# Kernel tuning notes

Hardware: AMD Instinct MI355X
Metric: run time of the kernel (lower is better)

## Reference

```python
import jax, jax.numpy as jnp
import numpy as np

E, F, H = 8, 5632, 2048
T = 8192


def setup_inputs() -> dict:
    key = jax.random.key(0)
    k1, k2, k3, k4 = jax.random.split(key, 4)
    s_w = 1.0 / np.sqrt(H)
    return {
        "expert_idx": 3,
        "hidden_states": jax.random.normal(k1, (T, H), dtype=jnp.float32),
        "fc1_1": jax.random.normal(k2, (E, F, H), dtype=jnp.float32) * s_w,
        "fc1_2": jax.random.normal(k3, (E, F, H), dtype=jnp.float32) * s_w,
        "fc2": jax.random.normal(k4, (E, H, F), dtype=jnp.float32) * (1.0 / np.sqrt(F)),
    }


def reference(expert_idx, hidden_states, fc1_1, fc1_2, fc2):
    # Select this expert's weights: [F,H], [F,H], [H,F]
    w1 = fc1_1[expert_idx]
    w2 = fc1_2[expert_idx]
    w3 = fc2[expert_idx]
    # SwiGLU FFN: silu(x @ w1^T) * (x @ w2^T) @ w3^T
    gate = jnp.einsum("th,fh->tf", hidden_states, w1)
    up = jnp.einsum("th,fh->tf", hidden_states, w2)
    fc1_out = jax.nn.silu(gate) * up  # [T, F]
    out = jnp.einsum("tf,hf->th", fc1_out, w3)  # [T, H]
    return out
```

## Files before the change

### kernel.cpp

```cpp
#include <hip/hip_runtime.h>
#include <hip/hip_bf16.h>

#define T_DIM 8192
#define H_DIM 2048
#define F_DIM 5632

typedef __attribute__((ext_vector_type(4))) float f32x4;
typedef __attribute__((ext_vector_type(8))) short bf16x8;

static __device__ __forceinline__ void gload16(const void* g, void* l) {
    __builtin_amdgcn_global_load_lds(
        (const __attribute__((address_space(1))) void*)g,
        (__attribute__((address_space(3))) void*)l,
        16, 0, 0);
}

static __device__ __forceinline__ unsigned short f2bf(float f) {
    unsigned int u = __float_as_uint(f);
    u += 0x7fffu + ((u >> 16) & 1u);
    return (unsigned short)(u >> 16);
}

__global__ __launch_bounds__(256)
void cvt_x(const float* __restrict__ src, unsigned short* __restrict__ dst, long n)
{
    const long stride = (long)gridDim.x * blockDim.x;
    for (long i = (long)blockIdx.x * blockDim.x + threadIdx.x; i * 4 < n; i += stride) {
        const float4 v = *(const float4*)(src + i * 4);
        ushort4 o;
        o.x = f2bf(v.x); o.y = f2bf(v.y); o.z = f2bf(v.z); o.w = f2bf(v.w);
        *(ushort4*)(dst + i * 4) = o;
    }
}

__global__ __launch_bounds__(256)
void cvt_w(const float* __restrict__ w1, const float* __restrict__ w2,
           const float* __restrict__ w3, const int* __restrict__ eidx,
           unsigned short* __restrict__ W12, unsigned short* __restrict__ W3b)
{
    const long seg = (long)F_DIM * H_DIM;
    const long e   = (long)(*eidx);
    const long nchunks = 3 * seg / 4;
    const long stride = (long)gridDim.x * blockDim.x;
    for (long i = (long)blockIdx.x * blockDim.x + threadIdx.x; i < nchunks; i += stride) {
        const long t = i * 4;
        const int  s = (int)(t / seg);
        const long o = t - (long)s * seg;
        const float4 v = *(const float4*)((s == 0 ? w1 : s == 1 ? w2 : w3) + e * seg + o);
        ushort4 ov;
        ov.x = f2bf(v.x); ov.y = f2bf(v.y); ov.z = f2bf(v.z); ov.w = f2bf(v.w);
        if (s == 2) {
            *(ushort4*)(W3b + o) = ov;
        } else {
            const long r   = o >> 11;
            const long col = o & 2047;
            const long R   = (r >> 4) * 32 + (r & 15) + (s == 1 ? 16 : 0);
            *(ushort4*)(W12 + R * 2048 + col) = ov;
        }
    }
}

static __device__ __forceinline__ void stage_half(const unsigned short* __restrict__ g,
                                                  long grow0, long ldk, long kb,
                                                  unsigned short* l, int t, int i0)
{
    const int r  = t >> 3;
    const int cc = ((t & 7) ^ (r & 7)) << 3;
    #pragma unroll
    for (int ii = i0; ii < i0 + 2; ++ii)
        gload16(g + (grow0 + ii * 64 + r) * ldk + kb + cc,
                l + ii * 4096 + t * 8);
}

static __device__ __forceinline__ bf16x8 ldsfrag(const unsigned short* base,
                                                 int row, int kk, int q)
{
    return *(const bf16x8*)(base + row * 64 + (((kk * 4 + q) ^ (row & 7)) << 3));
}

__global__ __launch_bounds__(512, 4)
void gemm_fc1(const unsigned short* __restrict__ X,
              const unsigned short* __restrict__ W12,
              unsigned short* __restrict__ Hout)
{
    constexpr int NK = H_DIM / 64;

    __shared__ __align__(16) unsigned short sAll[40960];

    const int tid  = threadIdx.x;
    const int lane = tid & 63;
    const int wid  = tid >> 6;
    const int wm   = wid >> 2;
    const int wn   = wid & 3;
    const int q    = lane >> 4;
    const int lr   = lane & 15;

    const int bid = blockIdx.x;
    const int x   = bid & 7;
    const int ii  = bid >> 3;
    const int bn  = ii >> 2;
    const int bm  = x * 4 + (ii & 3);

    const long arow0 = (long)bm * 256;
    const long brow0 = (long)bn * 128;

    unsigned short* sB = sAll + 32768;

    f32x4 acc[8][2] = {};

    stage_half(X,   arow0, H_DIM, 0, sAll, tid, 0);
    stage_half(X,   arow0, H_DIM, 0, sAll, tid, 2);
    stage_half(W12, brow0, H_DIM, 0, sB,   tid, 0);

    for (int j = 0; j < NK; ++j) {
        unsigned short* la = sAll + (j & 1) * 16384;

        if (j + 1 < NK) {
            unsigned short* na = sAll + ((j + 1) & 1) * 16384;
            stage_half(X, arow0, H_DIM, (long)(j + 1) * 64, na, tid, 0);
            stage_half(X, arow0, H_DIM, (long)(j + 1) * 64, na, tid, 2);
            asm volatile("s_waitcnt vmcnt(4)" ::: "memory");
        } else {
            asm volatile("s_waitcnt vmcnt(0)" ::: "memory");
        }
        __builtin_amdgcn_s_barrier();

        bf16x8 bf[2][2];
        #pragma unroll
        for (int nb = 0; nb < 2; ++nb)
            #pragma unroll
            for (int kk = 0; kk < 2; ++kk)
                bf[nb][kk] = ldsfrag(sB, wn * 32 + nb * 16 + lr, kk, q);

        bf16x8 af0[4][2];
        #pragma unroll
        for (int mi = 0; mi < 4; ++mi)
            #pragma unroll
            for (int kk = 0; kk < 2; ++kk)
                af0[mi][kk] = ldsfrag(la, wm * 128 + mi * 16 + lr, kk, q);
        __builtin_amdgcn_s_barrier();
        __builtin_amdgcn_s_setprio(1);
        #pragma unroll
        for (int mi = 0; mi < 4; ++mi)
            #pragma unroll
            for (int nb = 0; nb < 2; ++nb)
                #pragma unroll
                for (int kk = 0; kk < 2; ++kk)
                    acc[mi][nb] = __builtin_amdgcn_mfma_f32_16x16x32_bf16(
                        af0[mi][kk], bf[nb][kk], acc[mi][nb], 0, 0, 0);
        __builtin_amdgcn_s_setprio(0);

        bf16x8 af1[4][2];
        #pragma unroll
        for (int mi = 0; mi < 4; ++mi)
            #pragma unroll
            for (int kk = 0; kk < 2; ++kk)
                af1[mi][kk] = ldsfrag(la, wm * 128 + (mi + 4) * 16 + lr, kk, q);
        if (j + 1 < NK)
            stage_half(W12, brow0, H_DIM, (long)(j + 1) * 64, sB, tid, 0);
        __builtin_amdgcn_s_barrier();
        __builtin_amdgcn_s_setprio(1);
        #pragma unroll
        for (int mi = 0; mi < 4; ++mi)
            #pragma unroll
            for (int nb = 0; nb < 2; ++nb)
                #pragma unroll
                for (int kk = 0; kk < 2; ++kk)
                    acc[mi + 4][nb] = __builtin_amdgcn_mfma_f32_16x16x32_bf16(
                        af1[mi][kk], bf[nb][kk], acc[mi + 4][nb], 0, 0, 0);
        __builtin_amdgcn_s_setprio(0);
    }

    const long orow = (long)bm * 256 + wm * 128;
    const long ocol = (long)bn * 64 + wn * 16 + lr;
    #pragma unroll
    for (int mi = 0; mi < 8; ++mi)
        #pragma unroll
        for (int r = 0; r < 4; ++r) {
            const float g = acc[mi][0][r];
            const float u = acc[mi][1][r];
            const float h = __fdividef(g, 1.0f + __expf(-g)) * u;
            Hout[(orow + mi * 16 + q * 4 + r) * (long)F_DIM + ocol] = f2bf(h);
        }
}

#define PHASE_BODY(p, STAGE_STMT)                                              \
    {                                                                          \
        bf16x8 af[2][2];                                                       \
        _Pragma("unroll")                                                      \
        for (int l_ = 0; l_ < 2; ++l_)                                         \
            _Pragma("unroll")                                                  \
            for (int kk = 0; kk < 2; ++kk)                                     \
                af[l_][kk] = ldsfrag(la, wm * 128 + (p) * 32 + l_ * 16 + lr, kk, q); \
        STAGE_STMT;                                                            \
        __builtin_amdgcn_s_barrier();                                          \
        __builtin_amdgcn_s_setprio(1);                                         \
        _Pragma("unroll")                                                      \
        for (int l_ = 0; l_ < 2; ++l_)                                         \
            _Pragma("unroll")                                                  \
            for (int ni = 0; ni < 4; ++ni)                                     \
                _Pragma("unroll")                                              \
                for (int kk = 0; kk < 2; ++kk)                                 \
                    acc[(p) * 2 + l_][ni] = __builtin_amdgcn_mfma_f32_16x16x32_bf16( \
                        af[l_][kk], bf[ni][kk], acc[(p) * 2 + l_][ni], 0, 0, 0);     \
        __builtin_amdgcn_s_setprio(0);                                         \
        __builtin_amdgcn_s_barrier();                                          \
    }

__global__ __launch_bounds__(512, 2)
void gemm_out(const unsigned short* __restrict__ A,
              const unsigned short* __restrict__ B,
              float* __restrict__ Out)
{
    constexpr int NK  = F_DIM / 64;
    constexpr int NBN = H_DIM / 256;

    __shared__ __align__(16) unsigned short sAll[4 * 16384];

    const int tid  = threadIdx.x;
    const int lane = tid & 63;
    const int wid  = tid >> 6;
    const int wm   = wid >> 2;
    const int wn   = wid & 3;
    const int q    = lane >> 4;
    const int lr   = lane & 15;

    const int nwg = gridDim.x;
    const int bid = blockIdx.x;
    const int cpx = nwg >> 3;
    const int swz = (bid & 7) * cpx + (bid >> 3);
    const int bm  = swz / NBN;
    const int bn  = swz % NBN;

    const long arow0 = (long)bm * 256;
    const long brow0 = (long)bn * 256;

    f32x4 acc[8][4] = {};

    stage_half(A, arow0, F_DIM, 0,  sAll,          tid, 0);
    stage_half(A, arow0, F_DIM, 0,  sAll,          tid, 2);
    stage_half(B, brow0, F_DIM, 0,  sAll + 16384,  tid, 0);
    stage_half(B, brow0, F_DIM, 0,  sAll + 16384,  tid, 2);
    stage_half(B, brow0, F_DIM, 64, sAll + 49152,  tid, 0);
    stage_half(B, brow0, F_DIM, 64, sAll + 49152,  tid, 2);

    for (int j = 0; j < NK; ++j) {
        unsigned short* la = sAll + (j & 1) * 32768;
        unsigned short* lb = la + 16384;

        if (j + 1 < NK) {
            unsigned short* na = sAll + ((j + 1) & 1) * 32768;
            stage_half(A, arow0, F_DIM, (long)(j + 1) * 64, na, tid, 0);
            stage_half(A, arow0, F_DIM, (long)(j + 1) * 64, na, tid, 2);
            asm volatile("s_waitcnt vmcnt(8)" ::: "memory");
        } else {
            asm volatile("s_waitcnt vmcnt(0)" ::: "memory");
        }
        __builtin_amdgcn_s_barrier();

        bf16x8 bf[4][2];
        #pragma unroll
        for (int ni = 0; ni < 4; ++ni)
            #pragma unroll
            for (int kk = 0; kk < 2; ++kk)
                bf[ni][kk] = ldsfrag(lb, wn * 64 + ni * 16 + lr, kk, q);

        PHASE_BODY(0, {})
        PHASE_BODY(1, { if (j + 2 < NK) stage_half(B, brow0, F_DIM, (long)(j + 2) * 64, lb, tid, 0); })
        PHASE_BODY(2, { if (j + 2 < NK) stage_half(B, brow0, F_DIM, (long)(j + 2) * 64, lb, tid, 2); })
        PHASE_BODY(3, {})
    }

    const long orow = (long)bm * 256 + wm * 128;
    const long ocol = (long)bn * 256 + wn * 64;
    #pragma unroll
    for (int mi = 0; mi < 8; ++mi)
        #pragma unroll
        for (int ni = 0; ni < 4; ++ni)
            #pragma unroll
            for (int r = 0; r < 4; ++r)
                Out[(orow + mi * 16 + q * 4 + r) * (long)H_DIM + (ocol + ni * 16 + lr)]
                    = acc[mi][ni][r];
}

extern "C" void kernel_launch(void* const* d_in, const int* in_sizes, int n_in,
                              void* d_out, int out_size, void* d_ws, size_t ws_size,
                              hipStream_t stream)
{
    const int*   eidx = (const int*)d_in[0];
    const float* x    = (const float*)d_in[1];
    const float* w1   = (const float*)d_in[2];
    const float* w2   = (const float*)d_in[3];
    const float* w3   = (const float*)d_in[4];
    float* out = (float*)d_out;

    const size_t SZ_X = (size_t)T_DIM * H_DIM;
    const size_t SZ_W = (size_t)F_DIM * H_DIM;

    unsigned short* Xb  = (unsigned short*)d_ws;
    unsigned short* W12 = Xb  + SZ_X;
    unsigned short* W3b = W12 + 2 * SZ_W;
    unsigned short* Hb  = W3b + SZ_W;

    cvt_x<<<2048, 256, 0, stream>>>(x, Xb, (long)SZ_X);
    cvt_w<<<2048, 256, 0, stream>>>(w1, w2, w3, eidx, W12, W3b);

    gemm_fc1<<<2816, 512, 0, stream>>>(Xb, W12, Hb);
    gemm_out<<<(T_DIM / 256) * (H_DIM / 256), 512, 0, stream>>>(Hb, W3b, out);
}
```

Measured before the change: 545.8 us.

## Reshape fc1 GEMM tile to 128x256 with wider B tile per wave

Changes the fc1 gate/up GEMM block tile from 256 rows of X by 128 interleaved weight rows to 128 rows of X by 256 weight rows. Each wave now computes a 64x64 sub-tile instead of 128x32, and shared memory drops from 80KB to 64KB. The block-index mapping, staging counts and wait counts are adjusted to match, and extra barriers are added after each MFMA phase. The aim is a more square per-wave tile, better LDS fragment reuse and higher occupancy. The added barriers and the changed grid mapping could cost synchronisation time and L2 locality.

```diff
diff --git a/kernel.cpp b/kernel.cpp
--- a/kernel.cpp
+++ b/kernel.cpp
@@ -85,7 +85,7 @@
 {
     constexpr int NK = H_DIM / 64;
 
-    __shared__ __align__(16) unsigned short sAll[40960];
+    __shared__ __align__(16) unsigned short sAll[32768];
 
     const int tid  = threadIdx.x;
     const int lane = tid & 63;
@@ -98,90 +98,100 @@
     const int bid = blockIdx.x;
     const int x   = bid & 7;
     const int ii  = bid >> 3;
-    const int bn  = ii >> 2;
-    const int bm  = x * 4 + (ii & 3);
-
-    const long arow0 = (long)bm * 256;
-    const long brow0 = (long)bn * 128;
-
-    unsigned short* sB = sAll + 32768;
-
-    f32x4 acc[8][2] = {};
+    const int bn  = ii >> 3;
+    const int bm  = x * 8 + (ii & 7);
+
+    const long arow0 = (long)bm * 128;
+    const long brow0 = (long)bn * 256;
+
+    unsigned short* sB = sAll + 16384;
+
+    f32x4 acc[4][4] = {};
 
     stage_half(X,   arow0, H_DIM, 0, sAll, tid, 0);
-    stage_half(X,   arow0, H_DIM, 0, sAll, tid, 2);
     stage_half(W12, brow0, H_DIM, 0, sB,   tid, 0);
+    stage_half(W12, brow0, H_DIM, 0, sB,   tid, 2);
 
     for (int j = 0; j < NK; ++j) {
-        unsigned short* la = sAll + (j & 1) * 16384;
+        unsigned short* la = sAll + (j & 1) * 8192;
 
         if (j + 1 < NK) {
-            unsigned short* na = sAll + ((j + 1) & 1) * 16384;
+            unsigned short* na = sAll + ((j + 1) & 1) * 8192;
             stage_half(X, arow0, H_DIM, (long)(j + 1) * 64, na, tid, 0);
-            stage_half(X, arow0, H_DIM, (long)(j + 1) * 64, na, tid, 2);
-            asm volatile("s_waitcnt vmcnt(4)" ::: "memory");
+            asm volatile("s_waitcnt vmcnt(2)" ::: "memory");
         } else {
             asm volatile("s_waitcnt vmcnt(0)" ::: "memory");
         }
         __builtin_amdgcn_s_barrier();
 
-        bf16x8 bf[2][2];
+        bf16x8 bf[4][2];
         #pragma unroll
-        for (int nb = 0; nb < 2; ++nb)
+        for (int nf = 0; nf < 4; ++nf)
             #pragma unroll
             for (int kk = 0; kk < 2; ++kk)
-                bf[nb][kk] = ldsfrag(sB, wn * 32 + nb * 16 + lr, kk, q);
-
-        bf16x8 af0[4][2];
-        #pragma unroll
-        for (int mi = 0; mi < 4; ++mi)
-            #pragma unroll
-            for (int kk = 0; kk < 2; ++kk)
-                af0[mi][kk] = ldsfrag(la, wm * 128 + mi * 16 + lr, kk, q);
-        __builtin_amdgcn_s_barrier();
-        __builtin_amdgcn_s_setprio(1);
-        #pragma unroll
-        for (int mi = 0; mi < 4; ++mi)
-            #pragma unroll
-            for (int nb = 0; nb < 2; ++nb)
+                bf[nf][kk] = ldsfrag(sB, wn * 64 + nf * 16 + lr, kk, q);
+
+        {
+            bf16x8 af[2][2];
+            #pragma unroll
+            for (int mi = 0; mi < 2; ++mi)
                 #pragma unroll
                 for (int kk = 0; kk < 2; ++kk)
-                    acc[mi][nb] = __builtin_amdgcn_mfma_f32_16x16x32_bf16(
-                        af0[mi][kk], bf[nb][kk], acc[mi][nb], 0, 0, 0);
-        __builtin_amdgcn_s_setprio(0);
-
-        bf16x8 af1[4][2];
-        #pragma unroll
-        for (int mi = 0; mi < 4; ++mi)
-            #pragma unroll
-            for (int kk = 0; kk < 2; ++kk)
-                af1[mi][kk] = ldsfrag(la, wm * 128 + (mi + 4) * 16 + lr, kk, q);
-        if (j + 1 < NK)
-            stage_half(W12, brow0, H_DIM, (long)(j + 1) * 64, sB, tid, 0);
-        __builtin_amdgcn_s_barrier();
-        __builtin_amdgcn_s_setprio(1);
-        #pragma unroll
-        for (int mi = 0; mi < 4; ++mi)
-            #pragma unroll
-            for (int nb = 0; nb < 2; ++nb)
+                    af[mi][kk] = ldsfrag(la, wm * 64 + mi * 16 + lr, kk, q);
+            __builtin_amdgcn_s_barrier();
+            __builtin_amdgcn_s_setprio(1);
+            #pragma unroll
+            for (int mi = 0; mi < 2; ++mi)
+                #pragma unroll
+                for (int nf = 0; nf < 4; ++nf)
+                    #pragma unroll
+                    for (int kk = 0; kk < 2; ++kk)
+                        acc[mi][nf] = __builtin_amdgcn_mfma_f32_16x16x32_bf16(
+                            af[mi][kk], bf[nf][kk], acc[mi][nf], 0, 0, 0);
+            __builtin_amdgcn_s_setprio(0);
+            __builtin_amdgcn_s_barrier();
+        }
+
+        {
+            bf16x8 af[2][2];
+            #pragma unroll
+            for (int mi = 0; mi < 2; ++mi)
                 #pragma unroll
                 for (int kk = 0; kk < 2; ++kk)
-                    acc[mi + 4][nb] = __builtin_amdgcn_mfma_f32_16x16x32_bf16(
-                        af1[mi][kk], bf[nb][kk], acc[mi + 4][nb], 0, 0, 0);
-        __builtin_amdgcn_s_setprio(0);
-    }
-
-    const long orow = (long)bm * 256 + wm * 128;
-    const long ocol = (long)bn * 64 + wn * 16 + lr;
+                    af[mi][kk] = ldsfrag(la, wm * 64 + (mi + 2) * 16 + lr, kk, q);
+            if (j + 1 < NK) {
+                stage_half(W12, brow0, H_DIM, (long)(j + 1) * 64, sB, tid, 0);
+                stage_half(W12, brow0, H_DIM, (long)(j + 1) * 64, sB, tid, 2);
+            }
+            __builtin_amdgcn_s_barrier();
+            __builtin_amdgcn_s_setprio(1);
+            #pragma unroll
+            for (int mi = 0; mi < 2; ++mi)
+                #pragma unroll
+                for (int nf = 0; nf < 4; ++nf)
+                    #pragma unroll
+                    for (int kk = 0; kk < 2; ++kk)
+                        acc[mi + 2][nf] = __builtin_amdgcn_mfma_f32_16x16x32_bf16(
+                            af[mi][kk], bf[nf][kk], acc[mi + 2][nf], 0, 0, 0);
+            __builtin_amdgcn_s_setprio(0);
+            __builtin_amdgcn_s_barrier();
+        }
+    }
+
+    const long orow = (long)bm * 128 + wm * 64;
+    const long ocolb = (long)bn * 128 + wn * 32;
     #pragma unroll
-    for (int mi = 0; mi < 8; ++mi)
+    for (int mi = 0; mi < 4; ++mi)
         #pragma unroll
-        for (int r = 0; r < 4; ++r) {
-            const float g = acc[mi][0][r];
-            const float u = acc[mi][1][r];
-            const float h = __fdividef(g, 1.0f + __expf(-g)) * u;
-            Hout[(orow + mi * 16 + q * 4 + r) * (long)F_DIM + ocol] = f2bf(h);
-        }
+        for (int nj = 0; nj < 2; ++nj)
+            #pragma unroll
+            for (int r = 0; r < 4; ++r) {
+                const float g = acc[mi][2 * nj][r];
+                const float u = acc[mi][2 * nj + 1][r];
+                const float h = __fdividef(g, 1.0f + __expf(-g)) * u;
+                Hout[(orow + mi * 16 + q * 4 + r) * (long)F_DIM +
+                     (ocolb + nj * 16 + lr)] = f2bf(h);
+            }
 }
 
 #define PHASE_BODY(p, STAGE_STMT)                                              \
```

Result: no change. 553.5 us (+1.4%).

## Switch fc1 GEMM to 32x32x16 MFMA with 4x2 wave layout

Applied to the files above, without the earlier changes.

The fc1 gate/up GEMM now uses 32x32x16 bf16 MFMA tiles instead of 16x16x32, and the eight waves are rearranged as a 4x2 grid, each owning 64 rows by 64 interleaved gate/up columns. The W12 interleave is widened from 16-row to 32-row groups so that each 32-column fragment pair lines up as gate and up for the fused SiLU epilogue. Larger MFMA tiles need fewer LDS fragment reads per FLOP and fewer MFMA issues. The cost is a different accumulator register layout, an extra barrier after each phase, and possibly more register pressure.

```diff
diff --git a/kernel.cpp b/kernel.cpp
--- a/kernel.cpp
+++ b/kernel.cpp
@@ -5,8 +5,9 @@
 #define H_DIM 2048
 #define F_DIM 5632
 
-typedef __attribute__((ext_vector_type(4))) float f32x4;
-typedef __attribute__((ext_vector_type(8))) short bf16x8;
+typedef __attribute__((ext_vector_type(4)))  float f32x4;
+typedef __attribute__((ext_vector_type(16))) float f32x16;
+typedef __attribute__((ext_vector_type(8)))  short bf16x8;
 
 static __device__ __forceinline__ void gload16(const void* g, void* l) {
     __builtin_amdgcn_global_load_lds(
@@ -54,7 +55,7 @@
         } else {
             const long r   = o >> 11;
             const long col = o & 2047;
-            const long R   = (r >> 4) * 32 + (r & 15) + (s == 1 ? 16 : 0);
+            const long R   = (r >> 5) * 64 + (r & 31) + (s == 1 ? 32 : 0);
             *(ushort4*)(W12 + R * 2048 + col) = ov;
         }
     }
@@ -72,10 +73,16 @@
                 l + ii * 4096 + t * 8);
 }
 
+static __device__ __forceinline__ bf16x8 ldsfragc(const unsigned short* base,
+                                                  int row, int c)
+{
+    return *(const bf16x8*)(base + row * 64 + ((c ^ (row & 7)) << 3));
+}
+
 static __device__ __forceinline__ bf16x8 ldsfrag(const unsigned short* base,
                                                  int row, int kk, int q)
 {
-    return *(const bf16x8*)(base + row * 64 + (((kk * 4 + q) ^ (row & 7)) << 3));
+    return ldsfragc(base, row, kk * 4 + q);
 }
 
 __global__ __launch_bounds__(512, 4)
@@ -90,10 +97,10 @@
     const int tid  = threadIdx.x;
     const int lane = tid & 63;
     const int wid  = tid >> 6;
-    const int wm   = wid >> 2;
-    const int wn   = wid & 3;
-    const int q    = lane >> 4;
-    const int lr   = lane & 15;
+    const int wm   = wid >> 1;
+    const int wn   = wid & 1;
+    const int l5   = lane & 31;
+    const int h    = lane >> 5;
 
     const int bid = blockIdx.x;
     const int x   = bid & 7;
@@ -106,7 +113,7 @@
 
     unsigned short* sB = sAll + 32768;
 
-    f32x4 acc[8][2] = {};
+    f32x16 acc[2][2] = {};
 
     stage_half(X,   arow0, H_DIM, 0, sAll, tid, 0);
     stage_half(X,   arow0, H_DIM, 0, sAll, tid, 2);
@@ -125,63 +132,63 @@
         }
         __builtin_amdgcn_s_barrier();
 
-        bf16x8 bf[2][2];
+        bf16x8 bf[2][4];
         #pragma unroll
-        for (int nb = 0; nb < 2; ++nb)
-            #pragma unroll
-            for (int kk = 0; kk < 2; ++kk)
-                bf[nb][kk] = ldsfrag(sB, wn * 32 + nb * 16 + lr, kk, q);
-
-        bf16x8 af0[4][2];
+        for (int nf = 0; nf < 2; ++nf)
+            #pragma unroll
+            for (int s = 0; s < 4; ++s)
+                bf[nf][s] = ldsfragc(sB, wn * 64 + nf * 32 + l5, s * 2 + h);
+
+        {
+            bf16x8 af[4];
+            #pragma unroll
+            for (int s = 0; s < 4; ++s)
+                af[s] = ldsfragc(la, wm * 64 + l5, s * 2 + h);
+            __builtin_amdgcn_s_barrier();
+            __builtin_amdgcn_s_setprio(1);
+            #pragma unroll
+            for (int nf = 0; nf < 2; ++nf)
+                #pragma unroll
+                for (int s = 0; s < 4; ++s)
+                    acc[0][nf] = __builtin_amdgcn_mfma_f32_32x32x16_bf16(
+                        af[s], bf[nf][s], acc[0][nf], 0, 0, 0);
+            __builtin_amdgcn_s_setprio(0);
+            __builtin_amdgcn_s_barrier();
+        }
+
+        {
+            bf16x8 af[4];
+            #pragma unroll
+            for (int s = 0; s < 4; ++s)
+                af[s] = ldsfragc(la, wm * 64 + 32 + l5, s * 2 + h);
+            if (j + 1 < NK)
+                stage_half(W12, brow0, H_DIM, (long)(j + 1) * 64, sB, tid, 0);
+            __builtin_amdgcn_s_barrier();
+            __builtin_amdgcn_s_setprio(1);
+            #pragma unroll
+            for (int nf = 0; nf < 2; ++nf)
+                #pragma unroll
+                for (int s = 0; s < 4; ++s)
+                    acc[1][nf] = __builtin_amdgcn_mfma_f32_32x32x16_bf16(
+                        af[s], bf[nf][s], acc[1][nf], 0, 0, 0);
+            __builtin_amdgcn_s_setprio(0);
+            __builtin_amdgcn_s_barrier();
+        }
+    }
+
+    const long col = (long)bn * 64 + wn * 32 + l5;
+    #pragma unroll
+    for (int mi = 0; mi < 2; ++mi) {
+        const long rowb = (long)bm * 256 + wm * 64 + mi * 32 + 4 * h;
         #pragma unroll
-        for (int mi = 0; mi < 4; ++mi)
-            #pragma unroll
-            for (int kk = 0; kk < 2; ++kk)
-                af0[mi][kk] = ldsfrag(la, wm * 128 + mi * 16 + lr, kk, q);
-        __builtin_amdgcn_s_barrier();
-        __builtin_amdgcn_s_setprio(1);
-        #pragma unroll
-        for (int mi = 0; mi < 4; ++mi)
-            #pragma unroll
-            for (int nb = 0; nb < 2; ++nb)
-                #pragma unroll
-                for (int kk = 0; kk < 2; ++kk)
-                    acc[mi][nb] = __builtin_amdgcn_mfma_f32_16x16x32_bf16(
-                        af0[mi][kk], bf[nb][kk], acc[mi][nb], 0, 0, 0);
-        __builtin_amdgcn_s_setprio(0);
-
-        bf16x8 af1[4][2];
-        #pragma unroll
-        for (int mi = 0; mi < 4; ++mi)
-            #pragma unroll
-            for (int kk = 0; kk < 2; ++kk)
-                af1[mi][kk] = ldsfrag(la, wm * 128 + (mi + 4) * 16 + lr, kk, q);
-        if (j + 1 < NK)
-            stage_half(W12, brow0, H_DIM, (long)(j + 1) * 64, sB, tid, 0);
-        __builtin_amdgcn_s_barrier();
-        __builtin_amdgcn_s_setprio(1);
-        #pragma unroll
-        for (int mi = 0; mi < 4; ++mi)
-            #pragma unroll
-            for (int nb = 0; nb < 2; ++nb)
-                #pragma unroll
-                for (int kk = 0; kk < 2; ++kk)
-                    acc[mi + 4][nb] = __builtin_amdgcn_mfma_f32_16x16x32_bf16(
-                        af1[mi][kk], bf[nb][kk], acc[mi + 4][nb], 0, 0, 0);
-        __builtin_amdgcn_s_setprio(0);
-    }
-
-    const long orow = (long)bm * 256 + wm * 128;
-    const long ocol = (long)bn * 64 + wn * 16 + lr;
-    #pragma unroll
-    for (int mi = 0; mi < 8; ++mi)
-        #pragma unroll
-        for (int r = 0; r < 4; ++r) {
-            const float g = acc[mi][0][r];
-            const float u = acc[mi][1][r];
-            const float h = __fdividef(g, 1.0f + __expf(-g)) * u;
-            Hout[(orow + mi * 16 + q * 4 + r) * (long)F_DIM + ocol] = f2bf(h);
-        }
+        for (int reg = 0; reg < 16; ++reg) {
+            const long row = rowb + (reg & 3) + 8 * (reg >> 2);
+            const float g = acc[mi][0][reg];
+            const float u = acc[mi][1][reg];
+            const float hv = __fdividef(g, 1.0f + __expf(-g)) * u;
+            Hout[row * (long)F_DIM + col] = f2bf(hv);
+        }
+    }
 }
 
 #define PHASE_BODY(p, STAGE_STMT)                                              \
```

Result: slower. 657.9 us (+20.5%).

## Enlarge fc1 block tile to 256x256 with 1024 threads and double-buffered B

Applied to the files above, without the earlier changes.

The fused gate/up GEMM now uses 16 waves per block and a 256x256 output tile, doubling the weight rows per block and halving the grid. Both the X and W12 tiles are double-buffered in LDS, and the loads for the next K step are issued together. This replaces the old single-buffered B with its mid-iteration reload and extra barriers, leaving one barrier per K step. The aim is more operand reuse per LDS byte and less synchronization. The cost is 128 KB of LDS per block, which limits residency to one block per CU, plus coarser scheduling with fewer blocks.

```diff
diff --git a/kernel.cpp b/kernel.cpp
--- a/kernel.cpp
+++ b/kernel.cpp
@@ -72,26 +72,35 @@
                 l + ii * 4096 + t * 8);
 }
 
+static __device__ __forceinline__ void stage_q(const unsigned short* __restrict__ g,
+                                               long grow0, long ldk, long kb,
+                                               unsigned short* l, int t)
+{
+    const int r  = t >> 3;
+    const int cc = ((t & 7) ^ (r & 7)) << 3;
+    gload16(g + (grow0 + r) * ldk + kb + cc, l + t * 8);
+}
+
 static __device__ __forceinline__ bf16x8 ldsfrag(const unsigned short* base,
                                                  int row, int kk, int q)
 {
     return *(const bf16x8*)(base + row * 64 + (((kk * 4 + q) ^ (row & 7)) << 3));
 }
 
-__global__ __launch_bounds__(512, 4)
+__global__ __launch_bounds__(1024, 4)
 void gemm_fc1(const unsigned short* __restrict__ X,
               const unsigned short* __restrict__ W12,
               unsigned short* __restrict__ Hout)
 {
     constexpr int NK = H_DIM / 64;
 
-    __shared__ __align__(16) unsigned short sAll[40960];
+    __shared__ __align__(16) unsigned short sAll[65536];
 
     const int tid  = threadIdx.x;
     const int lane = tid & 63;
     const int wid  = tid >> 6;
-    const int wm   = wid >> 2;
-    const int wn   = wid & 3;
+    const int wm   = wid >> 3;
+    const int wn   = wid & 7;
     const int q    = lane >> 4;
     const int lr   = lane & 15;
 
@@ -102,23 +111,30 @@
     const int bm  = x * 4 + (ii & 3);
 
     const long arow0 = (long)bm * 256;
-    const long brow0 = (long)bn * 128;
-
-    unsigned short* sB = sAll + 32768;
+    const long brow0 = (long)bn * 256;
+
+    unsigned short* bufA = sAll;
+    unsigned short* bufB = sAll + 32768;
 
     f32x4 acc[8][2] = {};
 
-    stage_half(X,   arow0, H_DIM, 0, sAll, tid, 0);
-    stage_half(X,   arow0, H_DIM, 0, sAll, tid, 2);
-    stage_half(W12, brow0, H_DIM, 0, sB,   tid, 0);
+    stage_q(X,   arow0,       H_DIM, 0, bufA,        tid);
+    stage_q(X,   arow0 + 128, H_DIM, 0, bufA + 8192, tid);
+    stage_q(W12, brow0,       H_DIM, 0, bufB,        tid);
+    stage_q(W12, brow0 + 128, H_DIM, 0, bufB + 8192, tid);
 
     for (int j = 0; j < NK; ++j) {
-        unsigned short* la = sAll + (j & 1) * 16384;
+        unsigned short* la = bufA + (j & 1) * 16384;
+        unsigned short* lb = bufB + (j & 1) * 16384;
 
         if (j + 1 < NK) {
-            unsigned short* na = sAll + ((j + 1) & 1) * 16384;
-            stage_half(X, arow0, H_DIM, (long)(j + 1) * 64, na, tid, 0);
-            stage_half(X, arow0, H_DIM, (long)(j + 1) * 64, na, tid, 2);
+            unsigned short* na = bufA + ((j + 1) & 1) * 16384;
+            unsigned short* nb = bufB + ((j + 1) & 1) * 16384;
+            const long kbn = (long)(j + 1) * 64;
+            stage_q(X,   arow0,       H_DIM, kbn, na,        tid);
+            stage_q(X,   arow0 + 128, H_DIM, kbn, na + 8192, tid);
+            stage_q(W12, brow0,       H_DIM, kbn, nb,        tid);
+            stage_q(W12, brow0 + 128, H_DIM, kbn, nb + 8192, tid);
             asm volatile("s_waitcnt vmcnt(4)" ::: "memory");
         } else {
             asm volatile("s_waitcnt vmcnt(0)" ::: "memory");
@@ -127,52 +143,52 @@
 
         bf16x8 bf[2][2];
         #pragma unroll
-        for (int nb = 0; nb < 2; ++nb)
+        for (int nb_ = 0; nb_ < 2; ++nb_)
             #pragma unroll
             for (int kk = 0; kk < 2; ++kk)
-                bf[nb][kk] = ldsfrag(sB, wn * 32 + nb * 16 + lr, kk, q);
-
-        bf16x8 af0[4][2];
-        #pragma unroll
-        for (int mi = 0; mi < 4; ++mi)
-            #pragma unroll
-            for (int kk = 0; kk < 2; ++kk)
-                af0[mi][kk] = ldsfrag(la, wm * 128 + mi * 16 + lr, kk, q);
-        __builtin_amdgcn_s_barrier();
-        __builtin_amdgcn_s_setprio(1);
-        #pragma unroll
-        for (int mi = 0; mi < 4; ++mi)
-            #pragma unroll
-            for (int nb = 0; nb < 2; ++nb)
+                bf[nb_][kk] = ldsfrag(lb, wn * 32 + nb_ * 16 + lr, kk, q);
+
+        {
+            bf16x8 af[4][2];
+            #pragma unroll
+            for (int mi = 0; mi < 4; ++mi)
                 #pragma unroll
                 for (int kk = 0; kk < 2; ++kk)
-                    acc[mi][nb] = __builtin_amdgcn_mfma_f32_16x16x32_bf16(
-                        af0[mi][kk], bf[nb][kk], acc[mi][nb], 0, 0, 0);
-        __builtin_amdgcn_s_setprio(0);
-
-        bf16x8 af1[4][2];
-        #pragma unroll
-        for (int mi = 0; mi < 4; ++mi)
-            #pragma unroll
-            for (int kk = 0; kk < 2; ++kk)
-                af1[mi][kk] = ldsfrag(la, wm * 128 + (mi + 4) * 16 + lr, kk, q);
-        if (j + 1 < NK)
-            stage_half(W12, brow0, H_DIM, (long)(j + 1) * 64, sB, tid, 0);
-        __builtin_amdgcn_s_barrier();
-        __builtin_amdgcn_s_setprio(1);
-        #pragma unroll
-        for (int mi = 0; mi < 4; ++mi)
-            #pragma unroll
-            for (int nb = 0; nb < 2; ++nb)
+                    af[mi][kk] = ldsfrag(la, wm * 128 + mi * 16 + lr, kk, q);
+            __builtin_amdgcn_s_setprio(1);
+            #pragma unroll
+            for (int mi = 0; mi < 4; ++mi)
+                #pragma unroll
+                for (int nb_ = 0; nb_ < 2; ++nb_)
+                    #pragma unroll
+                    for (int kk = 0; kk < 2; ++kk)
+                        acc[mi][nb_] = __builtin_amdgcn_mfma_f32_16x16x32_bf16(
+                            af[mi][kk], bf[nb_][kk], acc[mi][nb_], 0, 0, 0);
+            __builtin_amdgcn_s_setprio(0);
+        }
+        {
+            bf16x8 af[4][2];
+            #pragma unroll
+            for (int mi = 0; mi < 4; ++mi)
                 #pragma unroll
                 for (int kk = 0; kk < 2; ++kk)
-                    acc[mi + 4][nb] = __builtin_amdgcn_mfma_f32_16x16x32_bf16(
-                        af1[mi][kk], bf[nb][kk], acc[mi + 4][nb], 0, 0, 0);
-        __builtin_amdgcn_s_setprio(0);
+                    af[mi][kk] = ldsfrag(la, wm * 128 + (mi + 4) * 16 + lr, kk, q);
+            __builtin_amdgcn_s_setprio(1);
+            #pragma unroll
+            for (int mi = 0; mi < 4; ++mi)
+                #pragma unroll
+                for (int nb_ = 0; nb_ < 2; ++nb_)
+                    #pragma unroll
+                    for (int kk = 0; kk < 2; ++kk)
+                        acc[mi + 4][nb_] = __builtin_amdgcn_mfma_f32_16x16x32_bf16(
+                            af[mi][kk], bf[nb_][kk], acc[mi + 4][nb_], 0, 0, 0);
+            __builtin_amdgcn_s_setprio(0);
+        }
+        __builtin_amdgcn_s_barrier();
     }
 
     const long orow = (long)bm * 256 + wm * 128;
-    const long ocol = (long)bn * 64 + wn * 16 + lr;
+    const long ocol = (long)bn * 128 + wn * 16 + lr;
     #pragma unroll
     for (int mi = 0; mi < 8; ++mi)
         #pragma unroll
@@ -305,6 +321,6 @@
     cvt_x<<<2048, 256, 0, stream>>>(x, Xb, (long)SZ_X);
     cvt_w<<<2048, 256, 0, stream>>>(w1, w2, w3, eidx, W12, W3b);
 
-    gemm_fc1<<<2816, 512, 0, stream>>>(Xb, W12, Hb);
+    gemm_fc1<<<1408, 1024, 0, stream>>>(Xb, W12, Hb);
     gemm_out<<<(T_DIM / 256) * (H_DIM / 256), 512, 0, stream>>>(Hb, W3b, out);
 }
```

Result: slower. 565.5 us (+3.6%).
